# Kernel optimization log

Measured on AMD Instinct MI355X. Metric: run time of the kernel, lower is better.

Reference implementation:

```python
import jax, jax.numpy as jnp
import numpy as np

R0 = 0.1          # radius threshold (init kwarg)
E = 33_554_432    # number of candidate pairs
N_NODES = 100_000 # node-id range for edge candidates


def setup_inputs() -> dict:
    key = jax.random.key(0)
    k1, k2 = jax.random.split(key)
    distanceVector = jax.random.uniform(k1, (E,), dtype=jnp.float32)
    edgeCands = jax.random.randint(k2, (E, 2), 0, N_NODES, dtype=jnp.int32)
    return {"distanceVector": distanceVector, "edgeCands": edgeCands}


def reference(distanceVector, edgeCands):
    # radiusGraphEdge_batched: elementwise threshold
    boolVector = distanceVector < R0
    # bool2edge_batched: stream compaction edgeCands[boolVector].
    # JAX/jit needs static shapes, so we compact into a fixed-size [E] buffer
    # padded with -1; n_edges gives the number of valid leading entries.
    n_edges = boolVector.sum()
    idx = jnp.nonzero(boolVector, size=E, fill_value=0)[0]  # [E] compacted indices
    eC = edgeCands[idx]                                     # [E, 2] gathered pairs
    valid = jnp.arange(E) < n_edges
    src = jnp.where(valid, eC[:, 0], -1)
    dst = jnp.where(valid, eC[:, 1], -1)
    return src, dst, n_edges
```

## Files before the change

kernel.cpp:

```cpp
#include <hip/hip_runtime.h>

#define R0 0.1f
#define BLOCK 256
#define CHUNK 4096

__global__ __launch_bounds__(BLOCK) void count_kernel(const float* __restrict__ dist,
                                                      int* __restrict__ blockCounts,
                                                      int E) {
    const int tid  = threadIdx.x;
    const int lane = tid & 63;
    const int wave = tid >> 6;
    const int E4   = E >> 2;
    const float4* d4 = reinterpret_cast<const float4*>(dist);

    int base4 = blockIdx.x * (CHUNK / 4) + tid;
    int cnt = 0;
#pragma unroll
    for (int k = 0; k < 4; ++k) {
        int i4 = base4 + k * BLOCK;
        if (i4 < E4) {
            float4 v = d4[i4];
            cnt += (v.x < R0) + (v.y < R0) + (v.z < R0) + (v.w < R0);
        }
    }
#pragma unroll
    for (int off = 32; off > 0; off >>= 1) cnt += __shfl_down(cnt, off, 64);
    __shared__ int wcnt[4];
    if (lane == 0) wcnt[wave] = cnt;
    __syncthreads();
    if (tid == 0) blockCounts[blockIdx.x] = wcnt[0] + wcnt[1] + wcnt[2] + wcnt[3];
}

__global__ __launch_bounds__(BLOCK) void scan_kernel(const int* __restrict__ blockCounts,
                                                     int* __restrict__ blockOffsets,
                                                     int nblocks,
                                                     int* __restrict__ totalOut) {
    const int tid  = threadIdx.x;
    const int lane = tid & 63;
    const int wave = tid >> 6;
    const int start = tid * 32;

    int cnts[32];
    int sum = 0;
#pragma unroll
    for (int j = 0; j < 32; ++j) {
        int b = start + j;
        int c = (b < nblocks) ? blockCounts[b] : 0;
        cnts[j] = c;
        sum += c;
    }
    int v = sum;
#pragma unroll
    for (int off = 1; off < 64; off <<= 1) {
        int n = __shfl_up(v, off, 64);
        if (lane >= off) v += n;
    }
    __shared__ int wtot[4], wpre[4];
    if (lane == 63) wtot[wave] = v;
    __syncthreads();
    if (tid == 0) {
        int r = 0;
        for (int w = 0; w < 4; ++w) { wpre[w] = r; r += wtot[w]; }
        *totalOut = r;
    }
    __syncthreads();
    int run = (v - sum) + wpre[wave];
#pragma unroll
    for (int j = 0; j < 32; ++j) {
        int b = start + j;
        if (b < nblocks) blockOffsets[b] = run;
        run += cnts[j];
    }
}

__global__ __launch_bounds__(BLOCK) void scatter_kernel(const float* __restrict__ dist,
                                                        const int2* __restrict__ edges,
                                                        const int* __restrict__ blockOffsets,
                                                        int* __restrict__ src,
                                                        int* __restrict__ dst,
                                                        int E) {
    const int tid  = threadIdx.x;
    const int lane = tid & 63;
    const int wave = tid >> 6;
    const int base = blockIdx.x * CHUNK;
    const int waveBase = base + wave * 1024;

    unsigned long long masks[16];
    int wcount = 0;
#pragma unroll
    for (int k = 0; k < 16; ++k) {
        int i = waveBase + k * 64 + lane;
        float d = (i < E) ? dist[i] : 1.0f;
        unsigned long long m = __ballot(d < R0);
        masks[k] = m;
        wcount += __popcll(m);
    }
    __shared__ int wtot[4], wpre[4];
    if (lane == 0) wtot[wave] = wcount;
    __syncthreads();
    if (tid == 0) {
        int r = 0;
        for (int w = 0; w < 4; ++w) { wpre[w] = r; r += wtot[w]; }
    }
    __syncthreads();

    int run = blockOffsets[blockIdx.x] + wpre[wave];
    const unsigned long long lanemask_lt = (lane == 0) ? 0ull : (~0ull >> (64 - lane));
#pragma unroll
    for (int k = 0; k < 16; ++k) {
        unsigned long long m = masks[k];
        int i = waveBase + k * 64 + lane;
        if ((m >> lane) & 1ull) {
            int pos = run + __popcll(m & lanemask_lt);
            int2 e = edges[i];
            src[pos] = e.x;
            dst[pos] = e.y;
        }
        run += __popcll(m);
    }
}

extern "C" void kernel_launch(void* const* d_in, const int* in_sizes, int n_in,
                              void* d_out, int out_size, void* d_ws, size_t ws_size,
                              hipStream_t stream) {
    const float* dist = (const float*)d_in[0];
    const int2*  edges = (const int2*)d_in[1];
    const int E = in_sizes[0];

    int* out   = (int*)d_out;
    int* src   = out;
    int* dst   = out + (size_t)E;
    int* total = out + (size_t)2 * E;

    const int nblocks = (E + CHUNK - 1) / CHUNK;
    int* blockCounts  = (int*)d_ws;
    int* blockOffsets = blockCounts + nblocks;

    hipMemsetAsync(d_out, 0xFF, (size_t)2 * E * sizeof(int), stream);

    count_kernel<<<nblocks, BLOCK, 0, stream>>>(dist, blockCounts, E);
    scan_kernel<<<1, BLOCK, 0, stream>>>(blockCounts, blockOffsets, nblocks, total);
    scatter_kernel<<<nblocks, BLOCK, 0, stream>>>(dist, edges, blockOffsets, src, dst, E);
}
```

Measured before the change: 551.0 us.

## Store ballot masks in count pass, drop memset, fill tail with -1 in scatter

```diff
diff --git a/kernel.cpp b/kernel.cpp
--- a/kernel.cpp
+++ b/kernel.cpp
@@ -4,31 +4,38 @@
 #define BLOCK 256
 #define CHUNK 4096
 
-__global__ __launch_bounds__(BLOCK) void count_kernel(const float* __restrict__ dist,
-                                                      int* __restrict__ blockCounts,
-                                                      int E) {
+typedef unsigned long long u64;
+typedef int int4v __attribute__((ext_vector_type(4)));
+
+__global__ __launch_bounds__(BLOCK) void count_mask_kernel(const float* __restrict__ dist,
+                                                           int* __restrict__ blockCounts,
+                                                           u64* __restrict__ maskBuf,
+                                                           int E) {
     const int tid  = threadIdx.x;
     const int lane = tid & 63;
     const int wave = tid >> 6;
     const int E4   = E >> 2;
     const float4* d4 = reinterpret_cast<const float4*>(dist);
+    const int blk = blockIdx.x;
 
-    int base4 = blockIdx.x * (CHUNK / 4) + tid;
-    int cnt = 0;
+    __shared__ int wcnt[4];
+    int mycnt = 0;
 #pragma unroll
     for (int k = 0; k < 4; ++k) {
-        int i4 = base4 + k * BLOCK;
-        if (i4 < E4) {
-            float4 v = d4[i4];
-            cnt += (v.x < R0) + (v.y < R0) + (v.z < R0) + (v.w < R0);
-        }
+        int i4 = blk * (CHUNK / 4) + k * BLOCK + tid;
+        float4 v = make_float4(1.f, 1.f, 1.f, 1.f);
+        if (i4 < E4) v = d4[i4];
+        u64 b0 = __ballot(v.x < R0);
+        u64 b1 = __ballot(v.y < R0);
+        u64 b2 = __ballot(v.z < R0);
+        u64 b3 = __ballot(v.w < R0);
+        u64* mptr = maskBuf + (((size_t)blk * 4 + k) * 4 + wave) * 4;
+        if (lane == 0) { mptr[0] = b0; mptr[1] = b1; mptr[2] = b2; mptr[3] = b3; }
+        mycnt += __popcll(b0) + __popcll(b1) + __popcll(b2) + __popcll(b3);
     }
-#pragma unroll
-    for (int off = 32; off > 0; off >>= 1) cnt += __shfl_down(cnt, off, 64);
-    __shared__ int wcnt[4];
-    if (lane == 0) wcnt[wave] = cnt;
+    if (lane == 0) wcnt[wave] = mycnt;
     __syncthreads();
-    if (tid == 0) blockCounts[blockIdx.x] = wcnt[0] + wcnt[1] + wcnt[2] + wcnt[3];
+    if (tid == 0) blockCounts[blk] = wcnt[0] + wcnt[1] + wcnt[2] + wcnt[3];
 }
 
 __global__ __launch_bounds__(BLOCK) void scan_kernel(const int* __restrict__ blockCounts,
@@ -73,57 +80,84 @@
     }
 }
 
-__global__ __launch_bounds__(BLOCK) void scatter_kernel(const float* __restrict__ dist,
-                                                        const int2* __restrict__ edges,
+__global__ __launch_bounds__(BLOCK) void scatter_kernel(const int2* __restrict__ edges,
+                                                        const u64* __restrict__ maskBuf,
                                                         const int* __restrict__ blockOffsets,
+                                                        const int* __restrict__ totalPtr,
                                                         int* __restrict__ src,
                                                         int* __restrict__ dst,
                                                         int E) {
     const int tid  = threadIdx.x;
     const int lane = tid & 63;
     const int wave = tid >> 6;
-    const int base = blockIdx.x * CHUNK;
-    const int waveBase = base + wave * 1024;
+    const int blk  = blockIdx.x;
+    const int base = blk * CHUNK;
+    const int nE   = *totalPtr;
 
-    unsigned long long masks[16];
-    int wcount = 0;
+    if (base + CHUNK > nE) {
+        const int4v m1 = {-1, -1, -1, -1};
 #pragma unroll
-    for (int k = 0; k < 16; ++k) {
-        int i = waveBase + k * 64 + lane;
-        float d = (i < E) ? dist[i] : 1.0f;
-        unsigned long long m = __ballot(d < R0);
-        masks[k] = m;
-        wcount += __popcll(m);
+        for (int t = 0; t < 4; ++t) {
+            int p = base + t * (BLOCK * 4) + tid * 4;
+            if (p >= nE) {
+                __builtin_nontemporal_store(m1, (int4v*)(src + p));
+                __builtin_nontemporal_store(m1, (int4v*)(dst + p));
+            } else if (p + 4 > nE) {
+#pragma unroll
+                for (int j = 0; j < 4; ++j)
+                    if (p + j >= nE) { src[p + j] = -1; dst[p + j] = -1; }
+            }
+        }
     }
-    __shared__ int wtot[4], wpre[4];
-    if (lane == 0) wtot[wave] = wcount;
-    __syncthreads();
-    if (tid == 0) {
-        int r = 0;
-        for (int w = 0; w < 4; ++w) { wpre[w] = r; r += wtot[w]; }
+
+    u64 b[4][4];
+    __shared__ int cnt[4][4];
+#pragma unroll
+    for (int k = 0; k < 4; ++k) {
+        const u64* mptr = maskBuf + (((size_t)blk * 4 + k) * 4 + wave) * 4;
+        b[k][0] = mptr[0]; b[k][1] = mptr[1]; b[k][2] = mptr[2]; b[k][3] = mptr[3];
+        if (lane == 0)
+            cnt[k][wave] = __popcll(b[k][0]) + __popcll(b[k][1]) +
+                           __popcll(b[k][2]) + __popcll(b[k][3]);
     }
     __syncthreads();
 
-    int run = blockOffsets[blockIdx.x] + wpre[wave];
-    const unsigned long long lanemask_lt = (lane == 0) ? 0ull : (~0ull >> (64 - lane));
+    int mypre[4];
+    {
+        int acc = 0;
 #pragma unroll
-    for (int k = 0; k < 16; ++k) {
-        unsigned long long m = masks[k];
-        int i = waveBase + k * 64 + lane;
-        if ((m >> lane) & 1ull) {
-            int pos = run + __popcll(m & lanemask_lt);
-            int2 e = edges[i];
-            src[pos] = e.x;
-            dst[pos] = e.y;
+        for (int kk = 0; kk < 4; ++kk) {
+#pragma unroll
+            for (int w = 0; w < 4; ++w) {
+                if (w == wave) mypre[kk] = acc;
+                acc += cnt[kk][w];
+            }
         }
-        run += __popcll(m);
+    }
+
+    const int run = blockOffsets[blk];
+    const u64 lt = (lane == 0) ? 0ull : (~0ull >> (64 - lane));
+#pragma unroll
+    for (int k = 0; k < 4; ++k) {
+        int rlane = run + mypre[k] +
+                    __popcll(b[k][0] & lt) + __popcll(b[k][1] & lt) +
+                    __popcll(b[k][2] & lt) + __popcll(b[k][3] & lt);
+        int e0 = base + k * 1024 + wave * 256 + lane * 4;
+        int f0 = (int)((b[k][0] >> lane) & 1ull);
+        int f1 = (int)((b[k][1] >> lane) & 1ull);
+        int f2 = (int)((b[k][2] >> lane) & 1ull);
+        int f3 = (int)((b[k][3] >> lane) & 1ull);
+        if (f0) { int2 e = edges[e0];     src[rlane] = e.x;            dst[rlane] = e.y; }
+        if (f1) { int2 e = edges[e0 + 1]; int p = rlane + f0;          src[p] = e.x; dst[p] = e.y; }
+        if (f2) { int2 e = edges[e0 + 2]; int p = rlane + f0 + f1;     src[p] = e.x; dst[p] = e.y; }
+        if (f3) { int2 e = edges[e0 + 3]; int p = rlane + f0 + f1 + f2; src[p] = e.x; dst[p] = e.y; }
     }
 }
 
 extern "C" void kernel_launch(void* const* d_in, const int* in_sizes, int n_in,
                               void* d_out, int out_size, void* d_ws, size_t ws_size,
                               hipStream_t stream) {
-    const float* dist = (const float*)d_in[0];
+    const float* dist  = (const float*)d_in[0];
     const int2*  edges = (const int2*)d_in[1];
     const int E = in_sizes[0];
 
@@ -133,12 +167,12 @@
     int* total = out + (size_t)2 * E;
 
     const int nblocks = (E + CHUNK - 1) / CHUNK;
+
     int* blockCounts  = (int*)d_ws;
     int* blockOffsets = blockCounts + nblocks;
+    u64* maskBuf      = (u64*)(blockOffsets + nblocks + 2);
 
-    hipMemsetAsync(d_out, 0xFF, (size_t)2 * E * sizeof(int), stream);
-
-    count_kernel<<<nblocks, BLOCK, 0, stream>>>(dist, blockCounts, E);
+    count_mask_kernel<<<nblocks, BLOCK, 0, stream>>>(dist, blockCounts, maskBuf, E);
     scan_kernel<<<1, BLOCK, 0, stream>>>(blockCounts, blockOffsets, nblocks, total);
-    scatter_kernel<<<nblocks, BLOCK, 0, stream>>>(dist, edges, blockOffsets, src, dst, E);
+    scatter_kernel<<<nblocks, BLOCK, 0, stream>>>(edges, maskBuf, blockOffsets, total, src, dst, E);
 }
```

Result: faster. 528.5 us (-4.1%).
